# Kernel tuning notes

Hardware: AMD Instinct MI355X
Metric: run time of the kernel (lower is better)

Reference implementation:

```python
import jax, jax.numpy as jnp
import numpy as np

B = 4096          # number of sampled constraints (batch)
H = 1024          # hidden_size
N_UNIT = 5
MAXD = 4          # max(DEPTHS)
TAU = 1.0
N_STEPS = N_UNIT * (1 + 2 * MAXD)  # 45
CLIST = np.linspace(10.0, 20.0, 5).astype(np.float32)
NSC = 11
DEPTH_VALS = np.array([2, 3, 4])
RATIO_VALS = np.array([3, 4, 6])
KS_VALS = np.array([3, 5, 7])


def setup_inputs() -> dict:
    key = jax.random.key(0)
    ks = jax.random.split(key, 20)
    def p(k, shape):
        return jax.random.uniform(k, shape, minval=-0.1, maxval=0.1, dtype=jnp.float32)
    return {
        'constraints': jax.random.uniform(ks[0], (B,), minval=10.0, maxval=20.0, dtype=jnp.float32),
        'superclass_id': 3,
        'gumbel_u': jax.random.uniform(ks[1], (N_STEPS, B, 3), minval=1e-6, maxval=1.0 - 1e-6, dtype=jnp.float32),
        'cond_emb': p(ks[2], (len(CLIST), H // 2)),
        'sc_emb': p(ks[3], (NSC, H // 2)),
        'depth_emb': p(ks[4], (3, H)),
        'ratio_emb': p(ks[5], (3, H)),
        'ks_emb': p(ks[6], (3, H)),
        'W_ih': p(ks[7], (4 * H, H)), 'b_ih': p(ks[8], (4 * H,)),
        'W_hh': p(ks[9], (4 * H, H)), 'b_hh': p(ks[10], (4 * H,)),
        'depth_W': p(ks[11], (3, H)), 'depth_b': p(ks[12], (3,)),
        'width_W': p(ks[13], (3, H)), 'width_b': p(ks[14], (3,)),
        'ks_W': p(ks[15], (3, H)), 'ks_b': p(ks[16], (3,)),
    }


def reference(constraints, superclass_id, gumbel_u, cond_emb, sc_emb, depth_emb, ratio_emb,
              ks_emb, W_ih, b_ih, W_hh, b_hh, depth_W, depth_b, width_W, width_b, ks_W, ks_b):
    clist = jnp.asarray(CLIST)
    # linear_interpolation: find bracketing interval for each constraint
    idx = jnp.clip(jnp.searchsorted(clist, constraints, side='right') - 1, 0, clist.shape[0] - 2)
    left, right = clist[idx], clist[idx + 1]
    w = ((right - constraints) / (right - left))[:, None]
    cemb = w * cond_emb[idx] + (1.0 - w) * cond_emb[idx + 1]          # [B, H/2]
    sce = jnp.broadcast_to(sc_emb[superclass_id], (constraints.shape[0], sc_emb.shape[1]))
    embed = jnp.concatenate([cemb, sce], axis=1)                       # [B, H]
    h = jnp.zeros((constraints.shape[0], H), embed.dtype)
    c = h

    def lstm(x, h, c):
        gates = x @ W_ih.T + b_ih + h @ W_hh.T + b_hh                  # [B, 4H]
        i, f, g, o = jnp.split(gates, 4, axis=-1)
        c2 = jax.nn.sigmoid(f) * c + jax.nn.sigmoid(i) * jnp.tanh(g)
        h2 = jax.nn.sigmoid(o) * jnp.tanh(c2)
        return h2, c2

    def gsample(logits, u):
        g = -jnp.log(-jnp.log(u))
        y_soft = jax.nn.softmax((logits + g) / TAU, axis=-1)
        onehot = jax.nn.one_hot(jnp.argmax(y_soft, -1), logits.shape[-1], dtype=y_soft.dtype)
        y_hard = onehot - jax.lax.stop_gradient(y_soft) + y_soft       # straight-through
        return jnp.argmax(y_hard, -1), y_soft, y_hard

    t = 0
    d_idx, d_probs, d_wbs = [], [], []
    r_idx, r_probs, r_wbs = [], [], []
    k_idx, k_probs, k_wbs = [], [], []
    for _unit in range(N_UNIT):
        h, c = lstm(embed, h, c)
        s, ys, yh = gsample(h @ depth_W.T + depth_b, gumbel_u[t]); t += 1
        d_idx.append(s); d_probs.append(ys); d_wbs.append(yh)
        embed = depth_emb[s]
        for _blk in range(MAXD):
            h, c = lstm(embed, h, c)
            s, ys, yh = gsample(h @ width_W.T + width_b, gumbel_u[t]); t += 1
            r_idx.append(s); r_probs.append(ys); r_wbs.append(yh)
            embed = ratio_emb[s]
            h, c = lstm(embed, h, c)
            s, ys, yh = gsample(h @ ks_W.T + ks_b, gumbel_u[t]); t += 1
            k_idx.append(s); k_probs.append(ys); k_wbs.append(yh)
            embed = ks_emb[s]

    depths = jnp.asarray(DEPTH_VALS)[jnp.stack(d_idx)]   # [5, B]
    ratios = jnp.asarray(RATIO_VALS)[jnp.stack(r_idx)]   # [20, B]
    kss = jnp.asarray(KS_VALS)[jnp.stack(k_idx)]         # [20, B]
    return (depths, ratios, kss,
            jnp.stack(d_wbs), jnp.stack(d_probs),
            jnp.stack(r_wbs), jnp.stack(r_probs),
            jnp.stack(k_wbs), jnp.stack(k_probs))
```

## Files before the change

### kernel.cpp

```cpp
#include <hip/hip_runtime.h>
#include <cmath>

namespace {

typedef _Float16 f16;
typedef f16 f16x8 __attribute__((ext_vector_type(8)));
typedef f16 f16x4 __attribute__((ext_vector_type(4)));
typedef float f32x4 __attribute__((ext_vector_type(4)));

constexpr int B  = 4096;
constexpr int H  = 1024;
constexpr int FH = 4 * H;
constexpr int NSTEPS = 45;
constexpr float INVS = 1.0f / 2048.0f;

__device__ __forceinline__ float sigf(float x) { return 1.0f / (1.0f + expf(-x)); }

struct HL { f16 h, l; };
__device__ __forceinline__ HL split16(float a) {
  float ah = (float)(f16)a;
  if (fabsf(a) < 6.1035156e-5f) ah = 0.0f;
  HL r; r.h = (f16)ah; r.l = (f16)((a - ah) * 2048.0f); return r;
}

__device__ __forceinline__ void async16(f16* lds_dst, const f16* gsrc) {
  __builtin_amdgcn_global_load_lds(
      (const __attribute__((address_space(1))) void*)gsrc,
      (__attribute__((address_space(3))) void*)lds_dst, 16, 0, 0);
}

__global__ void convertW_kernel(const float* __restrict__ W,
                                f16* __restrict__ Whi, f16* __restrict__ Wlo) {
  size_t i = ((size_t)blockIdx.x * 256 + threadIdx.x) * 4;
  float4 v = *(const float4*)(W + i);
  HL a = split16(v.x), b = split16(v.y), c = split16(v.z), d = split16(v.w);
  f16x4 hi = {a.h, b.h, c.h, d.h};
  f16x4 lo = {a.l, b.l, c.l, d.l};
  *(f16x4*)(Whi + i) = hi;
  *(f16x4*)(Wlo + i) = lo;
}

__global__ void precompute_kernel(
    const float* __restrict__ W_ih, const float* __restrict__ b_ih, const float* __restrict__ b_hh,
    const float* __restrict__ depth_emb, const float* __restrict__ ratio_emb, const float* __restrict__ ks_emb,
    const float* __restrict__ cond_emb, const float* __restrict__ sc_emb, const int* __restrict__ sid_p,
    float* __restrict__ tblD, float* __restrict__ tblR, float* __restrict__ tblK,
    float* __restrict__ condp, float* __restrict__ base0) {
  int j = blockIdx.x * blockDim.x + threadIdx.x;
  if (j >= FH) return;
  const float* wr = W_ih + (size_t)j * H;
  float aD0=0,aD1=0,aD2=0,aR0=0,aR1=0,aR2=0,aK0=0,aK1=0,aK2=0;
  for (int k = 0; k < H; ++k) {
    float w = wr[k];
    aD0 += depth_emb[k]       * w;
    aD1 += depth_emb[H + k]   * w;
    aD2 += depth_emb[2*H + k] * w;
    aR0 += ratio_emb[k]       * w;
    aR1 += ratio_emb[H + k]   * w;
    aR2 += ratio_emb[2*H + k] * w;
    aK0 += ks_emb[k]          * w;
    aK1 += ks_emb[H + k]      * w;
    aK2 += ks_emb[2*H + k]    * w;
  }
  int sid = sid_p[0];
  constexpr int HH = H / 2;
  float a0=0,a1=0,a2=0,a3=0,a4=0,aS=0;
  for (int k = 0; k < HH; ++k) {
    float w = wr[k];
    a0 += cond_emb[0*HH + k] * w;
    a1 += cond_emb[1*HH + k] * w;
    a2 += cond_emb[2*HH + k] * w;
    a3 += cond_emb[3*HH + k] * w;
    a4 += cond_emb[4*HH + k] * w;
    aS += sc_emb[sid*HH + k] * wr[HH + k];
  }
  float bias = b_ih[j] + b_hh[j];
  tblD[0*FH+j]=aD0+bias; tblD[1*FH+j]=aD1+bias; tblD[2*FH+j]=aD2+bias;
  tblR[0*FH+j]=aR0+bias; tblR[1*FH+j]=aR1+bias; tblR[2*FH+j]=aR2+bias;
  tblK[0*FH+j]=aK0+bias; tblK[1*FH+j]=aK1+bias; tblK[2*FH+j]=aK2+bias;
  condp[0*FH+j]=a0; condp[1*FH+j]=a1; condp[2*FH+j]=a2; condp[3*FH+j]=a3; condp[4*FH+j]=a4;
  base0[j] = aS + bias;
}

__global__ void step0_kernel(const float* __restrict__ constraints,
                             const float* __restrict__ condp, const float* __restrict__ base0,
                             f16* __restrict__ hhi, f16* __restrict__ hlo, float* __restrict__ c) {
  int idx = blockIdx.x * blockDim.x + threadIdx.x;
  int b = idx >> 10;
  int j = idx & (H - 1);
  float cv = constraints[b];
  int i0 = 0;
  if (cv >= 12.5f) i0 = 1;
  if (cv >= 15.0f) i0 = 2;
  if (cv >= 17.5f) i0 = 3;
  float right = 10.0f + 2.5f * (float)(i0 + 1);
  float w = (right - cv) / 2.5f;
  const float* c0 = condp + (size_t)i0 * FH;
  const float* c1 = c0 + FH;
  float iw = 1.0f - w;
  float xi = w*c0[j]       + iw*c1[j]       + base0[j];
  float xg = w*c0[2*H+j]   + iw*c1[2*H+j]   + base0[2*H+j];
  float xo = w*c0[3*H+j]   + iw*c1[3*H+j]   + base0[3*H+j];
  float cn = sigf(xi) * tanhf(xg);
  float hn = sigf(xo) * tanhf(cn);
  c[idx] = cn;
  HL s = split16(hn);
  hhi[idx] = s.h; hlo[idx] = s.l;
}

__global__ __launch_bounds__(256, 2) void lstm_step_mfma(
    const f16* __restrict__ hhi, const f16* __restrict__ hlo,
    f16* __restrict__ nhhi, f16* __restrict__ nhlo,
    float* __restrict__ cbuf,
    const f16* __restrict__ Whi, const f16* __restrict__ Wlo,
    const float* __restrict__ tbl, const int* __restrict__ sel) {
  __shared__ __align__(16) f16 lds[4 * 4096];
  f16* AHs = lds;
  f16* ALs = lds + 4096;
  f16* BHs = lds + 8192;
  f16* BLs = lds + 12288;

  const int tid  = threadIdx.x;
  const int lane = tid & 63;
  const int w    = tid >> 6;
  const int l15  = lane & 15;
  const int kph  = lane >> 4;
  const int b0   = blockIdx.y * 128;
  const int j0   = blockIdx.x * 32;

  f32x4 accH[4][4] = {};
  f32x4 accL[4][4] = {};

  const int srow = tid >> 2;
  const int cph  = tid & 3;

  for (int kt = 0; kt < H; kt += 32) {
    #pragma unroll
    for (int p = 0; p < 2; ++p) {
      int r  = p * 64 + srow;
      int cl = cph ^ (r & 3);
      int dst = p * 2048 + w * 512;
      const size_t asrc = (size_t)(b0 + r) * H + kt + cl * 8;
      async16(AHs + dst, hhi + asrc);
      async16(ALs + dst, hlo + asrc);
      int wrow = ((r >> 5) << 10) + j0 + (r & 31);
      const size_t bsrc = (size_t)wrow * H + kt + cl * 8;
      async16(BHs + dst, Whi + bsrc);
      async16(BLs + dst, Wlo + bsrc);
    }
    __syncthreads();

    f16x8 ah[4], al[4], bh[4], bl[4];
    #pragma unroll
    for (int mf = 0; mf < 4; ++mf) {
      int R = (w >> 1) * 64 + mf * 16 + l15;
      int off = R * 32 + (kph ^ (R & 3)) * 8;
      ah[mf] = *(const f16x8*)(AHs + off);
      al[mf] = *(const f16x8*)(ALs + off);
    }
    #pragma unroll
    for (int nf = 0; nf < 4; ++nf) {
      int R = nf * 32 + (w & 1) * 16 + l15;
      int off = R * 32 + (kph ^ (R & 3)) * 8;
      bh[nf] = *(const f16x8*)(BHs + off);
      bl[nf] = *(const f16x8*)(BLs + off);
    }
    #pragma unroll
    for (int mf = 0; mf < 4; ++mf) {
      #pragma unroll
      for (int nf = 0; nf < 4; ++nf) {
        accH[mf][nf] = __builtin_amdgcn_mfma_f32_16x16x32_f16(ah[mf], bh[nf], accH[mf][nf], 0, 0, 0);
        accL[mf][nf] = __builtin_amdgcn_mfma_f32_16x16x32_f16(ah[mf], bl[nf], accL[mf][nf], 0, 0, 0);
        accL[mf][nf] = __builtin_amdgcn_mfma_f32_16x16x32_f16(al[mf], bh[nf], accL[mf][nf], 0, 0, 0);
      }
    }
    __syncthreads();
  }

  #pragma unroll
  for (int mf = 0; mf < 4; ++mf) {
    #pragma unroll
    for (int r = 0; r < 4; ++r) {
      int b = b0 + (w >> 1) * 64 + mf * 16 + (lane >> 4) * 4 + r;
      int j = j0 + (w & 1) * 16 + l15;
      int s = sel[b];
      const float* t = tbl + (size_t)s * FH + j;
      float gi = accH[mf][0][r] + accL[mf][0][r] * INVS + t[0];
      float gf = accH[mf][1][r] + accL[mf][1][r] * INVS + t[H];
      float gg = accH[mf][2][r] + accL[mf][2][r] * INVS + t[2*H];
      float go = accH[mf][3][r] + accL[mf][3][r] * INVS + t[3*H];
      size_t off = (size_t)b * H + j;
      float cp = cbuf[off];
      float cn = sigf(gf) * cp + sigf(gi) * tanhf(gg);
      float hn = sigf(go) * tanhf(cn);
      cbuf[off] = cn;
      HL sp = split16(hn);
      nhhi[off] = sp.h;
      nhlo[off] = sp.l;
    }
  }
}

__global__ void sampler_kernel(const f16* __restrict__ hhi, const f16* __restrict__ hlo,
                               const float* __restrict__ selW, const float* __restrict__ selb,
                               const float* __restrict__ gu,
                               float* __restrict__ val_out, float* __restrict__ wb_out,
                               float* __restrict__ p_out,
                               float v0, float v1, float v2,
                               int* __restrict__ sel) {
  int wave = threadIdx.x >> 6;
  int lane = threadIdx.x & 63;
  int b = blockIdx.x * 4 + wave;
  const f16* hh = hhi + (size_t)b * H;
  const f16* hl = hlo + (size_t)b * H;
  float acc0 = 0, acc1 = 0, acc2 = 0;
  #pragma unroll
  for (int ch = 0; ch < 4; ++ch) {
    int k = ch * 256 + lane * 4;
    f16x4 vh = *(const f16x4*)(hh + k);
    f16x4 vl = *(const f16x4*)(hl + k);
    float x0 = (float)vh[0] + (float)vl[0] * INVS;
    float x1 = (float)vh[1] + (float)vl[1] * INVS;
    float x2 = (float)vh[2] + (float)vl[2] * INVS;
    float x3 = (float)vh[3] + (float)vl[3] * INVS;
    float4 w0 = *(const float4*)(selW + k);
    float4 w1 = *(const float4*)(selW + H + k);
    float4 w2 = *(const float4*)(selW + 2*H + k);
    acc0 += x0*w0.x + x1*w0.y + x2*w0.z + x3*w0.w;
    acc1 += x0*w1.x + x1*w1.y + x2*w1.z + x3*w1.w;
    acc2 += x0*w2.x + x1*w2.y + x2*w2.z + x3*w2.w;
  }
  #pragma unroll
  for (int off = 32; off > 0; off >>= 1) {
    acc0 += __shfl_xor(acc0, off);
    acc1 += __shfl_xor(acc1, off);
    acc2 += __shfl_xor(acc2, off);
  }
  if (lane == 0) {
    float y0 = acc0 + selb[0] - logf(-logf(gu[(size_t)b*3 + 0]));
    float y1 = acc1 + selb[1] - logf(-logf(gu[(size_t)b*3 + 1]));
    float y2 = acc2 + selb[2] - logf(-logf(gu[(size_t)b*3 + 2]));
    int s = 0;
    float best = y0;
    if (y1 > best) { s = 1; best = y1; }
    if (y2 > best) { s = 2; best = y2; }
    float e0 = expf(y0 - best), e1 = expf(y1 - best), e2 = expf(y2 - best);
    float inv = 1.0f / (e0 + e1 + e2);
    float p0 = e0 * inv, p1 = e1 * inv, p2 = e2 * inv;
    val_out[b] = (s == 0) ? v0 : ((s == 1) ? v1 : v2);
    wb_out[(size_t)b*3 + 0] = (s == 0) ? 1.0f : 0.0f;
    wb_out[(size_t)b*3 + 1] = (s == 1) ? 1.0f : 0.0f;
    wb_out[(size_t)b*3 + 2] = (s == 2) ? 1.0f : 0.0f;
    p_out[(size_t)b*3 + 0] = p0;
    p_out[(size_t)b*3 + 1] = p1;
    p_out[(size_t)b*3 + 2] = p2;
    sel[b] = s;
  }
}

}

extern "C" void kernel_launch(void* const* d_in, const int* in_sizes, int n_in,
                              void* d_out, int out_size, void* d_ws, size_t ws_size,
                              hipStream_t stream) {
  (void)in_sizes; (void)n_in; (void)out_size; (void)ws_size;
  const float* constraints = (const float*)d_in[0];
  const int*   sid         = (const int*)d_in[1];
  const float* gumbel      = (const float*)d_in[2];
  const float* cond_emb    = (const float*)d_in[3];
  const float* sc_emb      = (const float*)d_in[4];
  const float* depth_emb   = (const float*)d_in[5];
  const float* ratio_emb   = (const float*)d_in[6];
  const float* ks_emb      = (const float*)d_in[7];
  const float* W_ih        = (const float*)d_in[8];
  const float* W_hh        = (const float*)d_in[10];
  const float* b_ih        = (const float*)d_in[9];
  const float* b_hh        = (const float*)d_in[11];
  const float* depth_W     = (const float*)d_in[12];
  const float* depth_b     = (const float*)d_in[13];
  const float* width_W     = (const float*)d_in[14];
  const float* width_b     = (const float*)d_in[15];
  const float* ks_W        = (const float*)d_in[16];
  const float* ks_b        = (const float*)d_in[17];

  float* out = (float*)d_out;
  float* ws  = (float*)d_ws;

  float* cb    = ws;
  f16*   W16hi = (f16*)(cb + (size_t)B * H);
  f16*   W16lo = W16hi + (size_t)FH * H;
  f16*   hhiA  = W16lo + (size_t)FH * H;
  f16*   hloA  = hhiA + (size_t)B * H;
  f16*   hhiB  = hloA + (size_t)B * H;
  f16*   hloB  = hhiB + (size_t)B * H;
  float* tblD  = (float*)(hloB + (size_t)B * H);
  float* tblR  = tblD + 3 * FH;
  float* tblK  = tblR + 3 * FH;
  float* condp = tblK + 3 * FH;
  float* base0 = condp + 5 * FH;
  int*   sel   = (int*)(base0 + FH);

  convertW_kernel<<<(FH * H / 4) / 256, 256, 0, stream>>>(W_hh, W16hi, W16lo);
  precompute_kernel<<<FH / 256, 256, 0, stream>>>(
      W_ih, b_ih, b_hh, depth_emb, ratio_emb, ks_emb, cond_emb, sc_emb, sid,
      tblD, tblR, tblK, condp, base0);
  step0_kernel<<<(B * H) / 256, 256, 0, stream>>>(constraints, condp, base0, hhiA, hloA, cb);

  const float* selW_arr[3] = {depth_W, width_W, ks_W};
  const float* selb_arr[3] = {depth_b, width_b, ks_b};
  const float vals[3][3]   = {{2.f,3.f,4.f},{3.f,4.f,6.f},{3.f,5.f,7.f}};
  float* tbl_arr[3]        = {tblD, tblR, tblK};

  const size_t DEPTHS = 0,            RATIOS = (size_t)5*B,   KSS    = (size_t)25*B,
               DWBS   = (size_t)45*B, DPROBS = (size_t)60*B,
               RWBS   = (size_t)75*B, RPROBS = (size_t)135*B,
               KWBS   = (size_t)195*B, KPROBS = (size_t)255*B;

  f16* hhi_cur = hhiA; f16* hlo_cur = hloA;
  f16* hhi_nxt = hhiB; f16* hlo_nxt = hloB;
  for (int t = 0; t < NSTEPS; ++t) {
    if (t > 0) {
      int pt = (t - 1) % 9;
      int ptype = (pt == 0) ? 0 : ((pt & 1) ? 1 : 2);
      lstm_step_mfma<<<dim3(H / 32, B / 128), 256, 0, stream>>>(
          hhi_cur, hlo_cur, hhi_nxt, hlo_nxt, cb, W16hi, W16lo, tbl_arr[ptype], sel);
      f16* th = hhi_cur; hhi_cur = hhi_nxt; hhi_nxt = th;
      f16* tl = hlo_cur; hlo_cur = hlo_nxt; hlo_nxt = tl;
    }
    int r = t % 9, u = t / 9;
    int ty, row;
    float *valp, *wbp, *pp;
    if (r == 0)      { ty = 0; row = u;
      valp = out + DEPTHS + (size_t)row*B; wbp = out + DWBS + (size_t)row*B*3; pp = out + DPROBS + (size_t)row*B*3; }
    else if (r & 1)  { ty = 1; row = u*4 + (r-1)/2;
      valp = out + RATIOS + (size_t)row*B; wbp = out + RWBS + (size_t)row*B*3; pp = out + RPROBS + (size_t)row*B*3; }
    else             { ty = 2; row = u*4 + (r-2)/2;
      valp = out + KSS + (size_t)row*B;    wbp = out + KWBS + (size_t)row*B*3; pp = out + KPROBS + (size_t)row*B*3; }
    sampler_kernel<<<B / 4, 256, 0, stream>>>(
        hhi_cur, hlo_cur, selW_arr[ty], selb_arr[ty], gumbel + (size_t)t * B * 3,
        valp, wbp, pp, vals[ty][0], vals[ty][1], vals[ty][2], sel);
  }
}
```

Baseline: 5.708 ms.

## Double-buffer LSTM MFMA tiles, enlarge block, remap blocks per XCD, warp-parallel precompute

The LSTM step kernel now uses 512-thread blocks covering 256 batch rows, with a double-buffered LDS pipeline that prefetches the next K tile while MFMAs run on the current one. The LDS swizzle now also XORs in bits 2-3 of the row, and a 1D grid is remapped so blocks on the same XCD share W column tiles. The precompute kernel switches from one thread per output to one wavefront per output, using vector loads and shuffle reductions. The cost is twice the LDS per block, which may lower occupancy.

```diff
diff --git a/kernel.cpp b/kernel.cpp
--- a/kernel.cpp
+++ b/kernel.cpp
@@ -46,40 +46,57 @@
     const float* __restrict__ cond_emb, const float* __restrict__ sc_emb, const int* __restrict__ sid_p,
     float* __restrict__ tblD, float* __restrict__ tblR, float* __restrict__ tblK,
     float* __restrict__ condp, float* __restrict__ base0) {
-  int j = blockIdx.x * blockDim.x + threadIdx.x;
-  if (j >= FH) return;
+  const int w4   = threadIdx.x >> 6;
+  const int lane = threadIdx.x & 63;
+  const int j    = blockIdx.x * 4 + w4;
   const float* wr = W_ih + (size_t)j * H;
-  float aD0=0,aD1=0,aD2=0,aR0=0,aR1=0,aR2=0,aK0=0,aK1=0,aK2=0;
-  for (int k = 0; k < H; ++k) {
-    float w = wr[k];
-    aD0 += depth_emb[k]       * w;
-    aD1 += depth_emb[H + k]   * w;
-    aD2 += depth_emb[2*H + k] * w;
-    aR0 += ratio_emb[k]       * w;
-    aR1 += ratio_emb[H + k]   * w;
-    aR2 += ratio_emb[2*H + k] * w;
-    aK0 += ks_emb[k]          * w;
-    aK1 += ks_emb[H + k]      * w;
-    aK2 += ks_emb[2*H + k]    * w;
-  }
+  const int k = lane * 16;
+  float4 wv0 = *(const float4*)(wr + k);
+  float4 wv1 = *(const float4*)(wr + k + 4);
+  float4 wv2 = *(const float4*)(wr + k + 8);
+  float4 wv3 = *(const float4*)(wr + k + 12);
+
+  auto dot = [&](const float* e) -> float {
+    float4 e0 = *(const float4*)(e);
+    float4 e1 = *(const float4*)(e + 4);
+    float4 e2 = *(const float4*)(e + 8);
+    float4 e3 = *(const float4*)(e + 12);
+    return e0.x*wv0.x + e0.y*wv0.y + e0.z*wv0.z + e0.w*wv0.w
+         + e1.x*wv1.x + e1.y*wv1.y + e1.z*wv1.z + e1.w*wv1.w
+         + e2.x*wv2.x + e2.y*wv2.y + e2.z*wv2.z + e2.w*wv2.w
+         + e3.x*wv3.x + e3.y*wv3.y + e3.z*wv3.z + e3.w*wv3.w;
+  };
+
+  float a[15];
+  a[0] = dot(depth_emb + k);       a[1] = dot(depth_emb + H + k);   a[2] = dot(depth_emb + 2*H + k);
+  a[3] = dot(ratio_emb + k);       a[4] = dot(ratio_emb + H + k);   a[5] = dot(ratio_emb + 2*H + k);
+  a[6] = dot(ks_emb + k);          a[7] = dot(ks_emb + H + k);      a[8] = dot(ks_emb + 2*H + k);
+  a[9] = a[10] = a[11] = a[12] = a[13] = a[14] = 0.0f;
+  constexpr int HH = H / 2;
   int sid = sid_p[0];
-  constexpr int HH = H / 2;
-  float a0=0,a1=0,a2=0,a3=0,a4=0,aS=0;
-  for (int k = 0; k < HH; ++k) {
-    float w = wr[k];
-    a0 += cond_emb[0*HH + k] * w;
-    a1 += cond_emb[1*HH + k] * w;
-    a2 += cond_emb[2*HH + k] * w;
-    a3 += cond_emb[3*HH + k] * w;
-    a4 += cond_emb[4*HH + k] * w;
-    aS += sc_emb[sid*HH + k] * wr[HH + k];
-  }
-  float bias = b_ih[j] + b_hh[j];
-  tblD[0*FH+j]=aD0+bias; tblD[1*FH+j]=aD1+bias; tblD[2*FH+j]=aD2+bias;
-  tblR[0*FH+j]=aR0+bias; tblR[1*FH+j]=aR1+bias; tblR[2*FH+j]=aR2+bias;
-  tblK[0*FH+j]=aK0+bias; tblK[1*FH+j]=aK1+bias; tblK[2*FH+j]=aK2+bias;
-  condp[0*FH+j]=a0; condp[1*FH+j]=a1; condp[2*FH+j]=a2; condp[3*FH+j]=a3; condp[4*FH+j]=a4;
-  base0[j] = aS + bias;
+  if (lane < 32) {
+    a[9]  = dot(cond_emb + 0*HH + k);
+    a[10] = dot(cond_emb + 1*HH + k);
+    a[11] = dot(cond_emb + 2*HH + k);
+    a[12] = dot(cond_emb + 3*HH + k);
+    a[13] = dot(cond_emb + 4*HH + k);
+  } else {
+    a[14] = dot(sc_emb + sid*HH + (k - HH));
+  }
+  #pragma unroll
+  for (int i = 0; i < 15; ++i) {
+    #pragma unroll
+    for (int off = 32; off > 0; off >>= 1) a[i] += __shfl_xor(a[i], off);
+  }
+  if (lane == 0) {
+    float bias = b_ih[j] + b_hh[j];
+    tblD[0*FH+j]=a[0]+bias; tblD[1*FH+j]=a[1]+bias; tblD[2*FH+j]=a[2]+bias;
+    tblR[0*FH+j]=a[3]+bias; tblR[1*FH+j]=a[4]+bias; tblR[2*FH+j]=a[5]+bias;
+    tblK[0*FH+j]=a[6]+bias; tblK[1*FH+j]=a[7]+bias; tblK[2*FH+j]=a[8]+bias;
+    condp[0*FH+j]=a[9]; condp[1*FH+j]=a[10]; condp[2*FH+j]=a[11];
+    condp[3*FH+j]=a[12]; condp[4*FH+j]=a[13];
+    base0[j] = a[14] + bias;
+  }
 }
 
 __global__ void step0_kernel(const float* __restrict__ constraints,
@@ -108,62 +125,84 @@
   hhi[idx] = s.h; hlo[idx] = s.l;
 }
 
-__global__ __launch_bounds__(256, 2) void lstm_step_mfma(
+constexpr int BUFE = 24576;
+
+__device__ __forceinline__ void stage_tile(
+    f16* buf, const f16* hhi, const f16* hlo,
+    const f16* Whi, const f16* Wlo,
+    int b0, int j0, int kt, int tid, int w) {
+  int rs = tid >> 2;
+  int cs = tid & 3;
+  #pragma unroll
+  for (int p = 0; p < 2; ++p) {
+    int r  = p * 128 + rs;
+    int cl = cs ^ (r & 3) ^ ((r >> 2) & 3);
+    size_t src = (size_t)(b0 + r) * H + kt + cl * 8;
+    f16* dstA = buf + p * 4096 + w * 512;
+    async16(dstA, hhi + src);
+    async16(dstA + 8192, hlo + src);
+  }
+  {
+    int r  = rs;
+    int cl = cs ^ (r & 3) ^ ((r >> 2) & 3);
+    int wrow = ((r >> 5) << 10) + j0 + (r & 31);
+    size_t src = (size_t)wrow * H + kt + cl * 8;
+    f16* dstB = buf + 16384 + w * 512;
+    async16(dstB, Whi + src);
+    async16(dstB + 4096, Wlo + src);
+  }
+}
+
+__global__ __launch_bounds__(512, 2) void lstm_step_mfma(
     const f16* __restrict__ hhi, const f16* __restrict__ hlo,
     f16* __restrict__ nhhi, f16* __restrict__ nhlo,
     float* __restrict__ cbuf,
     const f16* __restrict__ Whi, const f16* __restrict__ Wlo,
     const float* __restrict__ tbl, const int* __restrict__ sel) {
-  __shared__ __align__(16) f16 lds[4 * 4096];
-  f16* AHs = lds;
-  f16* ALs = lds + 4096;
-  f16* BHs = lds + 8192;
-  f16* BLs = lds + 12288;
+  __shared__ __align__(16) f16 lds[2 * BUFE];
 
   const int tid  = threadIdx.x;
   const int lane = tid & 63;
   const int w    = tid >> 6;
+  const int wm   = w >> 1, wn = w & 1;
   const int l15  = lane & 15;
-  const int kph  = lane >> 4;
-  const int b0   = blockIdx.y * 128;
-  const int j0   = blockIdx.x * 32;
+  const int kq   = lane >> 4;
+
+  const int L   = blockIdx.x;
+  const int xcd = L & 7, seq = L >> 3;
+  const int jb  = (xcd << 2) + (seq & 3);
+  const int bb  = seq >> 2;
+  const int b0  = bb << 8;
+  const int j0  = jb << 5;
 
   f32x4 accH[4][4] = {};
   f32x4 accL[4][4] = {};
 
-  const int srow = tid >> 2;
-  const int cph  = tid & 3;
-
-  for (int kt = 0; kt < H; kt += 32) {
-    #pragma unroll
-    for (int p = 0; p < 2; ++p) {
-      int r  = p * 64 + srow;
-      int cl = cph ^ (r & 3);
-      int dst = p * 2048 + w * 512;
-      const size_t asrc = (size_t)(b0 + r) * H + kt + cl * 8;
-      async16(AHs + dst, hhi + asrc);
-      async16(ALs + dst, hlo + asrc);
-      int wrow = ((r >> 5) << 10) + j0 + (r & 31);
-      const size_t bsrc = (size_t)wrow * H + kt + cl * 8;
-      async16(BHs + dst, Whi + bsrc);
-      async16(BLs + dst, Wlo + bsrc);
-    }
-    __syncthreads();
-
+  stage_tile(lds, hhi, hlo, Whi, Wlo, b0, j0, 0, tid, w);
+  __syncthreads();
+
+  int cur = 0;
+  for (int kt = 0; kt < 32; ++kt) {
+    if (kt < 31)
+      stage_tile(lds + (cur ^ 1) * BUFE, hhi, hlo, Whi, Wlo, b0, j0, (kt + 1) * 32, tid, w);
+
+    const f16* bufc = lds + cur * BUFE;
     f16x8 ah[4], al[4], bh[4], bl[4];
     #pragma unroll
     for (int mf = 0; mf < 4; ++mf) {
-      int R = (w >> 1) * 64 + mf * 16 + l15;
-      int off = R * 32 + (kph ^ (R & 3)) * 8;
-      ah[mf] = *(const f16x8*)(AHs + off);
-      al[mf] = *(const f16x8*)(ALs + off);
+      int R = wm * 64 + mf * 16 + l15;
+      int c = kq ^ (R & 3) ^ ((R >> 2) & 3);
+      int off = R * 32 + c * 8;
+      ah[mf] = *(const f16x8*)(bufc + off);
+      al[mf] = *(const f16x8*)(bufc + 8192 + off);
     }
     #pragma unroll
     for (int nf = 0; nf < 4; ++nf) {
-      int R = nf * 32 + (w & 1) * 16 + l15;
-      int off = R * 32 + (kph ^ (R & 3)) * 8;
-      bh[nf] = *(const f16x8*)(BHs + off);
-      bl[nf] = *(const f16x8*)(BLs + off);
+      int R = nf * 32 + wn * 16 + l15;
+      int c = kq ^ (R & 3) ^ ((R >> 2) & 3);
+      int off = R * 32 + c * 8;
+      bh[nf] = *(const f16x8*)(bufc + 16384 + off);
+      bl[nf] = *(const f16x8*)(bufc + 20480 + off);
     }
     #pragma unroll
     for (int mf = 0; mf < 4; ++mf) {
@@ -175,14 +214,15 @@
       }
     }
     __syncthreads();
-  }
-
+    cur ^= 1;
+  }
+
+  const int j = j0 + wn * 16 + l15;
   #pragma unroll
   for (int mf = 0; mf < 4; ++mf) {
     #pragma unroll
     for (int r = 0; r < 4; ++r) {
-      int b = b0 + (w >> 1) * 64 + mf * 16 + (lane >> 4) * 4 + r;
-      int j = j0 + (w & 1) * 16 + l15;
+      int b = b0 + wm * 64 + mf * 16 + kq * 4 + r;
       int s = sel[b];
       const float* t = tbl + (size_t)s * FH + j;
       float gi = accH[mf][0][r] + accL[mf][0][r] * INVS + t[0];
@@ -273,8 +313,8 @@
   const float* ratio_emb   = (const float*)d_in[6];
   const float* ks_emb      = (const float*)d_in[7];
   const float* W_ih        = (const float*)d_in[8];
+  const float* b_ih        = (const float*)d_in[9];
   const float* W_hh        = (const float*)d_in[10];
-  const float* b_ih        = (const float*)d_in[9];
   const float* b_hh        = (const float*)d_in[11];
   const float* depth_W     = (const float*)d_in[12];
   const float* depth_b     = (const float*)d_in[13];
@@ -301,7 +341,7 @@
   int*   sel   = (int*)(base0 + FH);
 
   convertW_kernel<<<(FH * H / 4) / 256, 256, 0, stream>>>(W_hh, W16hi, W16lo);
-  precompute_kernel<<<FH / 256, 256, 0, stream>>>(
+  precompute_kernel<<<FH / 4, 256, 0, stream>>>(
       W_ih, b_ih, b_hh, depth_emb, ratio_emb, ks_emb, cond_emb, sc_emb, sid,
       tblD, tblR, tblK, condp, base0);
   step0_kernel<<<(B * H) / 256, 256, 0, stream>>>(constraints, condp, base0, hhiA, hloA, cb);
@@ -322,7 +362,7 @@
     if (t > 0) {
       int pt = (t - 1) % 9;
       int ptype = (pt == 0) ? 0 : ((pt & 1) ? 1 : 2);
-      lstm_step_mfma<<<dim3(H / 32, B / 128), 256, 0, stream>>>(
+      lstm_step_mfma<<<512, 512, 0, stream>>>(
           hhi_cur, hlo_cur, hhi_nxt, hlo_nxt, cb, W16hi, W16lo, tbl_arr[ptype], sel);
       f16* th = hhi_cur; hhi_cur = hhi_nxt; hhi_nxt = th;
       f16* tl = hlo_cur; hlo_cur = hlo_nxt; hlo_nxt = tl;
```

Result: faster. 5.207 ms (-8.8%).
